# Optimization experiments

Measured on AMD Instinct MI355X. Metric: run time of the kernel, lower is better.

Reference implementation:

```python
import jax, jax.numpy as jnp
import numpy as np

N_INST = 8      # number of instance labels present in target (== len(torch.unique(gt)))
DELTA_V = 0.5
ALPHA = 1.0
CLAMP_MAX = 100000.0


def setup_inputs() -> dict:
    key = jax.random.key(0)
    k1, k2 = jax.random.split(key)
    prediction = jax.random.normal(k1, (4, 16, 512, 512), dtype=jnp.float32)
    target = jax.random.randint(k2, (4, 512, 512), 0, N_INST)  # all labels 0..7 present whp
    return {"prediction": prediction, "target": target}


def _loss(prediction, target):
    B, nf, H, W = prediction.shape
    N = H * W
    pred = prediction.reshape(B, nf, N)                    # [B, nf, N]
    gt = target.reshape(B, N)                              # [B, N]
    # one-hot instance masks (unique sorted labels == arange(N_INST) by construction)
    mask = (gt[:, :, None] == jnp.arange(N_INST)[None, None, :]).astype(pred.dtype)  # [B, N, C]
    counts = mask.sum(axis=1)                              # [B, C] pixels per instance
    # per-instance means: sum of masked embeddings / counts
    means = jnp.einsum('bfn,bnc->bfc', pred, mask) / counts[:, None, :]  # [B, nf, C]
    # mu_expand - pred_masked = mask * (mu - pred); norm over feature dim
    diff = (means[:, :, None, :] - pred[:, :, :, None]) * mask[:, None, :, :]  # [B, nf, N, C]
    sq = jnp.sum(diff * diff, axis=1)                      # [B, N, C]
    # safe sqrt (zero where diff==0, matching torch.norm subgradient)
    d = jnp.where(sq > 0, jnp.sqrt(jnp.where(sq > 0, sq, 1.0)), 0.0)
    dist = jnp.clip(d - DELTA_V, 0.0, CLAMP_MAX) ** 2      # [B, N, C]
    # faithful to source: torch.sum(distance) is a full scalar reduce, then / counts, sum, / C
    l_var = dist.sum(axis=(1, 2)) * (1.0 / counts).sum(axis=1) / N_INST  # [B]
    return ALPHA * jnp.sum(l_var)


def reference(prediction, target):
    return _loss(prediction, target)
```

## Files before the change

### kernel.cpp

```cpp
#include <hip/hip_runtime.h>

#define NF   16
#define C    8
#define NB   4
#define NPIX (512*512)

#define SG      256
#define SCHUNK  (NPIX / SG)
#define SITERS  (SCHUNK / (64 * 4))

#define DG      256
#define DCHUNK  (NPIX / DG)

#define WS_PSUM 0
#define WS_PCNT (NB * SG * 128)
#define WS_MEAN (WS_PCNT + NB * SG * 8)
#define WS_INV  (WS_MEAN + NB * 128)
#define WS_POUT (WS_INV + NB)

__global__ __launch_bounds__(256) void sums_kernel(const float* __restrict__ pred,
                                                   const int* __restrict__ tgt,
                                                   float* __restrict__ ws) {
    const int tid  = threadIdx.x;
    const int lane = tid & 63;
    const int wave = tid >> 6;
    const int b    = blockIdx.y;
    const int f0   = wave * 4;

    const float* predb = pred + (size_t)b * NF * NPIX;
    const int*   tgtb  = tgt  + (size_t)b * NPIX;
    const int start = blockIdx.x * SCHUNK;

    float acc[4][8];
#pragma unroll
    for (int i = 0; i < 4; ++i)
#pragma unroll
        for (int c = 0; c < 8; ++c) acc[i][c] = 0.0f;
    float cnt[8];
#pragma unroll
    for (int c = 0; c < 8; ++c) cnt[c] = 0.0f;

#pragma unroll
    for (int it = 0; it < SITERS; ++it) {
        const int base = start + it * 256 + lane * 4;
        int4 lab = *(const int4*)(tgtb + base);
        float4 p[4];
#pragma unroll
        for (int fi = 0; fi < 4; ++fi)
            p[fi] = *(const float4*)(predb + (f0 + fi) * NPIX + base);

        const int labs[4] = { lab.x, lab.y, lab.z, lab.w };
#pragma unroll
        for (int px = 0; px < 4; ++px) {
            const int lv = labs[px];
            float m[8];
#pragma unroll
            for (int c = 0; c < 8; ++c) m[c] = (lv == c) ? 1.0f : 0.0f;
            if (wave == 0) {
#pragma unroll
                for (int c = 0; c < 8; ++c) cnt[c] += m[c];
            }
#pragma unroll
            for (int fi = 0; fi < 4; ++fi) {
                const float pv = (px == 0) ? p[fi].x :
                                 (px == 1) ? p[fi].y :
                                 (px == 2) ? p[fi].z : p[fi].w;
#pragma unroll
                for (int c = 0; c < 8; ++c) acc[fi][c] += m[c] * pv;
            }
        }
    }

#pragma unroll
    for (int off = 32; off > 0; off >>= 1) {
#pragma unroll
        for (int fi = 0; fi < 4; ++fi)
#pragma unroll
            for (int c = 0; c < 8; ++c)
                acc[fi][c] += __shfl_xor(acc[fi][c], off);
    }
    if (wave == 0) {
#pragma unroll
        for (int off = 32; off > 0; off >>= 1)
#pragma unroll
            for (int c = 0; c < 8; ++c)
                cnt[c] += __shfl_xor(cnt[c], off);
    }

    {
        float v = 0.0f;
#pragma unroll
        for (int fj = 0; fj < 4; ++fj)
#pragma unroll
            for (int cj = 0; cj < 8; ++cj)
                v = (lane == fj * 8 + cj) ? acc[fj][cj] : v;
        if (lane < 32)
            ws[WS_PSUM + ((size_t)(b * SG + blockIdx.x)) * 128 + f0 * 8 + lane] = v;
        if (wave == 0) {
            float cv = 0.0f;
#pragma unroll
            for (int cj = 0; cj < 8; ++cj)
                cv = (lane == 32 + cj) ? cnt[cj] : cv;
            if (lane >= 32 && lane < 40)
                ws[WS_PCNT + (b * SG + blockIdx.x) * 8 + (lane - 32)] = cv;
        }
    }
}

__global__ void means_kernel(float* __restrict__ ws) {
    __shared__ float scnt_p[32 * 8];
    __shared__ float scnt[8];
    __shared__ float smean[16 * 16];
    const int t = threadIdx.x, g = blockIdx.x, b = blockIdx.y;

    {
        const int c = t & 7, part = t >> 3;
        float s = 0.0f;
#pragma unroll
        for (int i = 0; i < 8; ++i)
            s += ws[WS_PCNT + (b * SG + part * 8 + i) * 8 + c];
        scnt_p[part * 8 + c] = s;
    }
    __syncthreads();
    if (t < 8) {
        float s = 0.0f;
        for (int p = 0; p < 32; ++p) s += scnt_p[p * 8 + t];
        scnt[t] = s;
    }
    __syncthreads();

    {
        const int fcl = t & 15, part = t >> 4;
        const int fc = g * 16 + fcl;
        float s = 0.0f;
#pragma unroll
        for (int i = 0; i < 16; ++i)
            s += ws[WS_PSUM + (size_t)(b * SG + part * 16 + i) * 128 + fc];
        smean[part * 16 + fcl] = s;
    }
    __syncthreads();
    if (t < 16) {
        float s = 0.0f;
        for (int p = 0; p < 16; ++p) s += smean[p * 16 + t];
        const int fc = g * 16 + t;
        ws[WS_MEAN + b * 128 + fc] = s / scnt[fc & 7];
    }
    if (g == 0 && t == 0) {
        float iv = 0.0f;
#pragma unroll
        for (int c = 0; c < 8; ++c) iv += 1.0f / scnt[c];
        ws[WS_INV + b] = iv;
    }
}

__global__ __launch_bounds__(256) void dist_kernel(const float* __restrict__ pred,
                                                   const int* __restrict__ tgt,
                                                   const float* __restrict__ ws,
                                                   float* __restrict__ pout) {
    __shared__ float s_means[C * NF];
    __shared__ float s_red[4];
    const int tid = threadIdx.x;
    const int b   = blockIdx.y;
    if (tid < C * NF) s_means[tid] = ws[WS_MEAN + b * 128 + tid];
    const float invs = ws[WS_INV + b];
    __syncthreads();

    const float* predb = pred + (size_t)b * NF * NPIX;
    const int*   tgtb  = tgt  + (size_t)b * NPIX;

    const int base = blockIdx.x * DCHUNK + tid * 4;
    int4 lab = *(const int4*)(tgtb + base);
    float s0 = 0.f, s1 = 0.f, s2 = 0.f, s3 = 0.f;
#pragma unroll
    for (int f = 0; f < NF; ++f) {
        float4 p = *(const float4*)(predb + f * NPIX + base);
        float d0 = s_means[f * C + lab.x] - p.x;
        float d1 = s_means[f * C + lab.y] - p.y;
        float d2 = s_means[f * C + lab.z] - p.z;
        float d3 = s_means[f * C + lab.w] - p.w;
        s0 += d0 * d0; s1 += d1 * d1; s2 += d2 * d2; s3 += d3 * d3;
    }
    float t0 = fminf(fmaxf(sqrtf(s0) - 0.5f, 0.0f), 100000.0f);
    float t1 = fminf(fmaxf(sqrtf(s1) - 0.5f, 0.0f), 100000.0f);
    float t2 = fminf(fmaxf(sqrtf(s2) - 0.5f, 0.0f), 100000.0f);
    float t3 = fminf(fmaxf(sqrtf(s3) - 0.5f, 0.0f), 100000.0f);
    float acc = t0 * t0 + t1 * t1 + t2 * t2 + t3 * t3;

#pragma unroll
    for (int off = 32; off > 0; off >>= 1) acc += __shfl_down(acc, off);
    const int lane = tid & 63, wave = tid >> 6;
    if (lane == 0) s_red[wave] = acc;
    __syncthreads();
    if (tid == 0) {
        float tot = s_red[0] + s_red[1] + s_red[2] + s_red[3];
        pout[b * DG + blockIdx.x] = tot * invs * 0.125f;
    }
}

__global__ void final_kernel(const float* __restrict__ pout, float* __restrict__ out) {
    __shared__ float sr[8];
    const int t = threadIdx.x;
    float v = pout[t] + pout[t + 512];
#pragma unroll
    for (int off = 32; off > 0; off >>= 1) v += __shfl_xor(v, off);
    if ((t & 63) == 0) sr[t >> 6] = v;
    __syncthreads();
    if (t == 0) {
        float s = 0.0f;
#pragma unroll
        for (int i = 0; i < 8; ++i) s += sr[i];
        out[0] = s;
    }
}

extern "C" void kernel_launch(void* const* d_in, const int* in_sizes, int n_in,
                              void* d_out, int out_size, void* d_ws, size_t ws_size,
                              hipStream_t stream) {
    const float* pred = (const float*)d_in[0];
    const int*   tgt  = (const int*)d_in[1];
    float* out = (float*)d_out;
    float* ws  = (float*)d_ws;

    sums_kernel<<<dim3(SG, NB), dim3(256), 0, stream>>>(pred, tgt, ws);
    means_kernel<<<dim3(8, NB), dim3(256), 0, stream>>>(ws);
    dist_kernel<<<dim3(DG, NB), dim3(256), 0, stream>>>(pred, tgt, ws, ws + WS_POUT);
    final_kernel<<<dim3(1), dim3(512), 0, stream>>>(ws + WS_POUT, out);
}
```

Measured before the change: 116.7 us.

## Stage pred and label tiles into LDS via async global_load_lds in both passes

Both the sums and distance kernels now issue all of a block's global loads up front through the global-to-LDS direct load builtin, wait once at a barrier, then read from shared memory. The sums kernel is split into twice as many smaller blocks (512 pixels each), and the means kernel's partial reductions are widened to match. The goal is more memory-level parallelism and fewer dependent load stalls on a bandwidth-bound read of the 64 MB prediction tensor. In exchange it adds LDS pressure (up to ~68 KB per dist block, which limits occupancy), an extra barrier, and more partial sums to reduce.

```diff
diff --git a/kernel.cpp b/kernel.cpp
--- a/kernel.cpp
+++ b/kernel.cpp
@@ -5,31 +5,51 @@
 #define NB   4
 #define NPIX (512*512)
 
-#define SG      256
-#define SCHUNK  (NPIX / SG)
-#define SITERS  (SCHUNK / (64 * 4))
-
-#define DG      256
-#define DCHUNK  (NPIX / DG)
+#define SBPB   512
+#define SPX    512
+#define DBPB   256
+#define DPX    1024
 
 #define WS_PSUM 0
-#define WS_PCNT (NB * SG * 128)
-#define WS_MEAN (WS_PCNT + NB * SG * 8)
+#define WS_PCNT (NB * SBPB * 128)
+#define WS_MEAN (WS_PCNT + NB * SBPB * 8)
 #define WS_INV  (WS_MEAN + NB * 128)
 #define WS_POUT (WS_INV + NB)
+
+__device__ __forceinline__ void gload_lds16(const void* g, void* l) {
+    __builtin_amdgcn_global_load_lds((const __attribute__((address_space(1))) void*)g,
+                                     (__attribute__((address_space(3))) void*)l,
+                                     16, 0, 0);
+}
 
 __global__ __launch_bounds__(256) void sums_kernel(const float* __restrict__ pred,
                                                    const int* __restrict__ tgt,
                                                    float* __restrict__ ws) {
+    __shared__ float pred_s[NF * SPX];
+    __shared__ int   tgt_s[SPX];
     const int tid  = threadIdx.x;
     const int lane = tid & 63;
     const int wave = tid >> 6;
     const int b    = blockIdx.y;
+    const int blk  = blockIdx.x;
     const int f0   = wave * 4;
 
     const float* predb = pred + (size_t)b * NF * NPIX;
     const int*   tgtb  = tgt  + (size_t)b * NPIX;
-    const int start = blockIdx.x * SCHUNK;
+    const int S = blk * SPX;
+
+#pragma unroll
+    for (int fi = 0; fi < 4; ++fi)
+#pragma unroll
+        for (int half = 0; half < 2; ++half)
+            gload_lds16(predb + (f0 + fi) * NPIX + S + half * 256 + lane * 4,
+                        &pred_s[(f0 + fi) * SPX + half * 256]);
+    if (wave == 0) {
+#pragma unroll
+        for (int half = 0; half < 2; ++half)
+            gload_lds16(tgtb + S + half * 256 + lane * 4, &tgt_s[half * 256]);
+    }
+    __syncthreads();
 
     float acc[4][8];
 #pragma unroll
@@ -41,13 +61,13 @@
     for (int c = 0; c < 8; ++c) cnt[c] = 0.0f;
 
 #pragma unroll
-    for (int it = 0; it < SITERS; ++it) {
-        const int base = start + it * 256 + lane * 4;
-        int4 lab = *(const int4*)(tgtb + base);
+    for (int it = 0; it < SPX / 256; ++it) {
+        const int pxb = it * 256 + lane * 4;
+        int4 lab = *(const int4*)&tgt_s[pxb];
         float4 p[4];
 #pragma unroll
         for (int fi = 0; fi < 4; ++fi)
-            p[fi] = *(const float4*)(predb + (f0 + fi) * NPIX + base);
+            p[fi] = *(const float4*)&pred_s[(f0 + fi) * SPX + pxb];
 
         const int labs[4] = { lab.x, lab.y, lab.z, lab.w };
 #pragma unroll
@@ -95,14 +115,14 @@
             for (int cj = 0; cj < 8; ++cj)
                 v = (lane == fj * 8 + cj) ? acc[fj][cj] : v;
         if (lane < 32)
-            ws[WS_PSUM + ((size_t)(b * SG + blockIdx.x)) * 128 + f0 * 8 + lane] = v;
+            ws[WS_PSUM + ((size_t)(b * SBPB + blk)) * 128 + f0 * 8 + lane] = v;
         if (wave == 0) {
             float cv = 0.0f;
 #pragma unroll
             for (int cj = 0; cj < 8; ++cj)
                 cv = (lane == 32 + cj) ? cnt[cj] : cv;
             if (lane >= 32 && lane < 40)
-                ws[WS_PCNT + (b * SG + blockIdx.x) * 8 + (lane - 32)] = cv;
+                ws[WS_PCNT + (b * SBPB + blk) * 8 + (lane - 32)] = cv;
         }
     }
 }
@@ -117,8 +137,8 @@
         const int c = t & 7, part = t >> 3;
         float s = 0.0f;
 #pragma unroll
-        for (int i = 0; i < 8; ++i)
-            s += ws[WS_PCNT + (b * SG + part * 8 + i) * 8 + c];
+        for (int i = 0; i < 16; ++i)
+            s += ws[WS_PCNT + (b * SBPB + part * 16 + i) * 8 + c];
         scnt_p[part * 8 + c] = s;
     }
     __syncthreads();
@@ -134,8 +154,8 @@
         const int fc = g * 16 + fcl;
         float s = 0.0f;
 #pragma unroll
-        for (int i = 0; i < 16; ++i)
-            s += ws[WS_PSUM + (size_t)(b * SG + part * 16 + i) * 128 + fc];
+        for (int i = 0; i < 32; ++i)
+            s += ws[WS_PSUM + (size_t)(b * SBPB + part * 32 + i) * 128 + fc];
         smean[part * 16 + fcl] = s;
     }
     __syncthreads();
@@ -157,27 +177,46 @@
                                                    const int* __restrict__ tgt,
                                                    const float* __restrict__ ws,
                                                    float* __restrict__ pout) {
-    __shared__ float s_means[C * NF];
+    __shared__ float pred_s[NF * DPX];
+    __shared__ int   tgt_s[DPX];
+    __shared__ float s_mean[128];
     __shared__ float s_red[4];
-    const int tid = threadIdx.x;
-    const int b   = blockIdx.y;
-    if (tid < C * NF) s_means[tid] = ws[WS_MEAN + b * 128 + tid];
-    const float invs = ws[WS_INV + b];
-    __syncthreads();
+    const int tid  = threadIdx.x;
+    const int lane = tid & 63;
+    const int wave = tid >> 6;
+    const int b    = blockIdx.y;
+    const int blk  = blockIdx.x;
+    const int f0   = wave * 4;
 
     const float* predb = pred + (size_t)b * NF * NPIX;
     const int*   tgtb  = tgt  + (size_t)b * NPIX;
-
-    const int base = blockIdx.x * DCHUNK + tid * 4;
-    int4 lab = *(const int4*)(tgtb + base);
+    const int S = blk * DPX;
+
+#pragma unroll
+    for (int fi = 0; fi < 4; ++fi)
+#pragma unroll
+        for (int q = 0; q < 4; ++q)
+            gload_lds16(predb + (f0 + fi) * NPIX + S + q * 256 + lane * 4,
+                        &pred_s[(f0 + fi) * DPX + q * 256]);
+    if (wave == 0) {
+#pragma unroll
+        for (int q = 0; q < 4; ++q)
+            gload_lds16(tgtb + S + q * 256 + lane * 4, &tgt_s[q * 256]);
+    }
+    if (tid < 128) s_mean[tid] = ws[WS_MEAN + b * 128 + tid];
+    const float invs = ws[WS_INV + b];
+    __syncthreads();
+
+    const int pxb = tid * 4;
+    int4 lab = *(const int4*)&tgt_s[pxb];
     float s0 = 0.f, s1 = 0.f, s2 = 0.f, s3 = 0.f;
 #pragma unroll
     for (int f = 0; f < NF; ++f) {
-        float4 p = *(const float4*)(predb + f * NPIX + base);
-        float d0 = s_means[f * C + lab.x] - p.x;
-        float d1 = s_means[f * C + lab.y] - p.y;
-        float d2 = s_means[f * C + lab.z] - p.z;
-        float d3 = s_means[f * C + lab.w] - p.w;
+        float4 p = *(const float4*)&pred_s[f * DPX + pxb];
+        float d0 = s_mean[f * C + lab.x] - p.x;
+        float d1 = s_mean[f * C + lab.y] - p.y;
+        float d2 = s_mean[f * C + lab.z] - p.z;
+        float d3 = s_mean[f * C + lab.w] - p.w;
         s0 += d0 * d0; s1 += d1 * d1; s2 += d2 * d2; s3 += d3 * d3;
     }
     float t0 = fminf(fmaxf(sqrtf(s0) - 0.5f, 0.0f), 100000.0f);
@@ -188,12 +227,11 @@
 
 #pragma unroll
     for (int off = 32; off > 0; off >>= 1) acc += __shfl_down(acc, off);
-    const int lane = tid & 63, wave = tid >> 6;
     if (lane == 0) s_red[wave] = acc;
     __syncthreads();
     if (tid == 0) {
         float tot = s_red[0] + s_red[1] + s_red[2] + s_red[3];
-        pout[b * DG + blockIdx.x] = tot * invs * 0.125f;
+        pout[b * DBPB + blk] = tot * invs * 0.125f;
     }
 }
 
@@ -221,8 +259,8 @@
     float* out = (float*)d_out;
     float* ws  = (float*)d_ws;
 
-    sums_kernel<<<dim3(SG, NB), dim3(256), 0, stream>>>(pred, tgt, ws);
+    sums_kernel<<<dim3(SBPB, NB), dim3(256), 0, stream>>>(pred, tgt, ws);
     means_kernel<<<dim3(8, NB), dim3(256), 0, stream>>>(ws);
-    dist_kernel<<<dim3(DG, NB), dim3(256), 0, stream>>>(pred, tgt, ws, ws + WS_POUT);
+    dist_kernel<<<dim3(DBPB, NB), dim3(256), 0, stream>>>(pred, tgt, ws, ws + WS_POUT);
     final_kernel<<<dim3(1), dim3(512), 0, stream>>>(ws + WS_POUT, out);
 }
```

Result: slower. 121.7 us (+4.3%).
